# Performance work log

Measured on AMD Instinct MI355X. Metric: run time of the kernel, lower is better.

The kernel has to match this reference:

```python
import math
import jax, jax.numpy as jnp
import numpy as np

TWO_PI = 2.0 * math.pi


def cyclic_catmull_rom(phase, num_cp):
    """Returns (indices [B,4] int32, weights [B,4] float)."""
    pos = jnp.remainder(phase, TWO_PI) * (num_cp / TWO_PI)
    base = jnp.floor(pos).astype(jnp.int32)
    t = pos - base.astype(pos.dtype)
    t2 = t * t
    t3 = t2 * t
    idx = jnp.stack([
        jnp.remainder(base - 1, num_cp),
        jnp.remainder(base, num_cp),
        jnp.remainder(base + 1, num_cp),
        jnp.remainder(base + 2, num_cp),
    ], axis=1)
    w = jnp.stack([
        -0.5 * t + t2 - 0.5 * t3,
        1.0 - 2.5 * t2 + 1.5 * t3,
        0.5 * t + 2.0 * t2 - 1.5 * t3,
        -0.5 * t2 + 0.5 * t3,
    ], axis=1)
    return idx, w


def setup_inputs() -> dict:
    key = jax.random.key(0)
    ks = jax.random.split(key, 10)
    B = 16384
    INPUT_DIM = 33          # phase + 32 state features
    STATE = 32
    EXP = 128               # expanded_input_dim
    PN = 8                  # phase_node_count
    C = 8                   # phase_control_points
    H1, H2 = 256, 256
    OUT = 16
    FIRST_IN = EXP + PN + STATE          # 168
    PF_IN = H1 + STATE                   # 288

    def xavier(k, shape):
        fan_out, fan_in = shape[-2], shape[-1]
        lim = math.sqrt(6.0 / (fan_in + fan_out))
        return jax.random.uniform(k, shape, jnp.float32, -lim, lim)

    return {
        "inputs": jax.random.normal(ks[0], (B, INPUT_DIM), jnp.float32),
        "exp_w": xavier(ks[1], (EXP, STATE)),
        "exp_b": jnp.zeros((EXP,), jnp.float32),
        "phase_node_cp": 0.02 * jax.random.normal(ks[2], (C, PN), jnp.float32),
        "w1": xavier(ks[3], (H1, FIRST_IN)),
        "b1": jnp.zeros((H1,), jnp.float32),
        "pf_w": xavier(ks[4], (C, H2, PF_IN)),
        "pf_b": jnp.zeros((C, H2), jnp.float32),
        "w_out": xavier(ks[5], (OUT, H2 + STATE)),
        "b_out": jnp.zeros((OUT,), jnp.float32),
    }


def reference(inputs, exp_w, exp_b, phase_node_cp, w1, b1, pf_w, pf_b, w_out, b_out):
    num_cp = pf_w.shape[0]
    phase = inputs[:, 0]
    state = inputs[:, 1:]                                  # [B, S]

    expanded = jax.nn.elu(state @ exp_w.T + exp_b)          # [B, EXP]

    idx, w = cyclic_catmull_rom(phase, num_cp)              # [B,4], [B,4]
    phase_nodes = jnp.sum(w[:, :, None] * phase_node_cp[idx], axis=1)  # [B, PN]

    h1 = jax.nn.elu(jnp.concatenate([expanded, phase_nodes, state], axis=1) @ w1.T + b1)
    h2_in = jnp.concatenate([h1, state], axis=1)            # [B, PF_IN]

    # Phase-functioned linear: compute matvec against every control matrix,
    # then gather + blend the 4 relevant ones (same math as blending weight
    # matrices first, by linearity; avoids the [B,4,OUT,IN] intermediate).
    z = jnp.einsum('bi,coi->bco', h2_in, pf_w)              # [B, C, H2]
    z4 = jnp.take_along_axis(z, idx[:, :, None], axis=1)    # [B, 4, H2]
    b4 = pf_b[idx]                                          # [B, 4, H2]
    h2 = jax.nn.elu(jnp.sum(w[:, :, None] * (z4 + b4), axis=1))

    return jnp.concatenate([h2, state], axis=1) @ w_out.T + b_out
```

## Files before the change

### kernel.cpp

```cpp
#include <hip/hip_runtime.h>
#include <math.h>

typedef short bf16x8 __attribute__((ext_vector_type(8)));
typedef float f32x4 __attribute__((ext_vector_type(4)));

#define MFMA16(a, b, c) __builtin_amdgcn_mfma_f32_16x16x32_bf16((a), (b), (c), 0, 0, 0)

#define TWO_PI_F 6.28318530717958647692f

#define PFW_OFF    0
#define PFW_ELEMS  (8 * 2 * 8 * 9 * 512)
#define W1_OFF     (PFW_OFF + PFW_ELEMS)
#define W1_ELEMS   (16 * 6 * 512)
#define EXPW_OFF   (W1_OFF + W1_ELEMS)
#define EXPW_ELEMS (8 * 512)
#define WOUT_OFF   (EXPW_OFF + EXPW_ELEMS)
#define WOUT_ELEMS (9 * 512)
#define TOTAL_ELEMS (WOUT_OFF + WOUT_ELEMS)

#define MAIN_THREADS 512
#define TILE_B 64

__device__ __forceinline__ unsigned short f2bf(float x) {
    unsigned int u = __float_as_uint(x);
    unsigned int r = u + 0x7fffu + ((u >> 16) & 1u);
    return (unsigned short)(r >> 16);
}

__device__ __forceinline__ float elu_f(float x) {
    return x > 0.0f ? x : (expf(x) - 1.0f);
}

__global__ __launch_bounds__(256) void prep_weights(
    const float* __restrict__ exp_w, const float* __restrict__ w1,
    const float* __restrict__ pf_w, const float* __restrict__ w_out,
    unsigned short* __restrict__ wsb)
{
    int i = blockIdx.x * blockDim.x + threadIdx.x;
    if (i >= TOTAL_ELEMS) return;
    float v;
    if (i < W1_OFF) {
        int f = i >> 9, e512 = i & 511;
        int ln = e512 >> 3, e = e512 & 7;
        int kgp = ln >> 4, cf = ln & 15;
        int kk = f % 9; int rest = f / 9;
        int n_t = rest & 7; int rest2 = rest >> 3;
        int half = rest2 & 1; int c = rest2 >> 1;
        int n = half * 128 + n_t * 16 + cf;
        int k = kk * 32 + kgp * 8 + e;
        v = pf_w[((size_t)(c * 256 + n)) * 288 + k];
    } else if (i < EXPW_OFF) {
        int j = i - W1_OFF;
        int f = j >> 9, e512 = j & 511;
        int ln = e512 >> 3, e = e512 & 7;
        int kgp = ln >> 4, cf = ln & 15;
        int kk = f % 6; int n16 = f / 6;
        int n = n16 * 16 + cf;
        int k = kk * 32 + kgp * 8 + e;
        v = (k < 168) ? w1[n * 168 + k] : 0.0f;
    } else if (i < WOUT_OFF) {
        int j = i - EXPW_OFF;
        int n16 = j >> 9; int e512 = j & 511;
        int ln = e512 >> 3, e = e512 & 7;
        int kgp = ln >> 4, cf = ln & 15;
        v = exp_w[(n16 * 16 + cf) * 32 + kgp * 8 + e];
    } else {
        int j = i - WOUT_OFF;
        int kk = j >> 9; int e512 = j & 511;
        int ln = e512 >> 3, e = e512 & 7;
        int kgp = ln >> 4, cf = ln & 15;
        int k = kk * 32 + kgp * 8 + e;
        v = w_out[cf * 288 + k];
    }
    wsb[i] = f2bf(v);
}

__global__ __launch_bounds__(MAIN_THREADS, 2) void pfnn_mfma(
    const float* __restrict__ inputs,
    const float* __restrict__ exp_b,
    const float* __restrict__ cp,
    const float* __restrict__ b1,
    const float* __restrict__ pf_b,
    const float* __restrict__ b_out,
    const unsigned short* __restrict__ wsb,
    float* __restrict__ out, int B)
{
    __shared__ __align__(16) unsigned short buf1[TILE_B * 296];
    __shared__ __align__(16) unsigned short buf2[TILE_B * 296];
    __shared__ float sWcT[8][TILE_B];

    const unsigned short* pfwb  = wsb + PFW_OFF;
    const unsigned short* w1b   = wsb + W1_OFF;
    const unsigned short* expwb = wsb + EXPW_OFF;
    const unsigned short* woutb = wsb + WOUT_OFF;

    const int t    = threadIdx.x;
    const int w    = t >> 6;
    const int lane = t & 63;
    const int cfr  = lane & 15;
    const int kg   = lane >> 4;
    const int b0   = blockIdx.x * TILE_B;

    for (int i = t; i < TILE_B * 32; i += MAIN_THREADS) {
        int row = i >> 5, j = i & 31;
        int grow = b0 + row;
        float v = (grow < B) ? inputs[(size_t)grow * 33 + 1 + j] : 0.0f;
        unsigned short bv = f2bf(v);
        buf1[row * 296 + 136 + j] = bv;
        buf1[row * 296 + 256 + j] = bv;
        buf2[row * 296 + 256 + j] = bv;
        buf1[row * 296 + 168 + j] = 0;
    }
    if (t < TILE_B) {
        int grow = b0 + t;
        float ph = (grow < B) ? inputs[(size_t)grow * 33] : 0.0f;
        float p = fmodf(ph, TWO_PI_F);
        if (p < 0.0f) p += TWO_PI_F;
        float pos = p * (8.0f / TWO_PI_F);
        int base = (int)floorf(pos);
        float tt = pos - (float)base;
        base &= 7;
        float t2 = tt * tt, t3 = t2 * tt;
        float cw0 = -0.5f * tt + t2 - 0.5f * t3;
        float cw1 = 1.0f - 2.5f * t2 + 1.5f * t3;
        float cw2 = 0.5f * tt + 2.0f * t2 - 1.5f * t3;
        float cw3 = -0.5f * t2 + 0.5f * t3;
        int i0 = (base + 7) & 7, i1 = base, i2 = (base + 1) & 7, i3 = (base + 2) & 7;
        #pragma unroll
        for (int c = 0; c < 8; ++c) sWcT[c][t] = 0.0f;
        sWcT[i0][t] += cw0;
        sWcT[i1][t] += cw1;
        sWcT[i2][t] += cw2;
        sWcT[i3][t] += cw3;
        #pragma unroll
        for (int j = 0; j < 8; ++j) {
            float pn = cw0 * cp[i0 * 8 + j] + cw1 * cp[i1 * 8 + j]
                     + cw2 * cp[i2 * 8 + j] + cw3 * cp[i3 * 8 + j];
            buf1[t * 296 + 128 + j] = f2bf(pn);
        }
    }
    __syncthreads();

    {
        const int n0 = w * 16;
        bf16x8 bw = *(const bf16x8*)(expwb + w * 512 + lane * 8);
        const f32x4 zero = {0.f, 0.f, 0.f, 0.f};
        f32x4 acc[4];
        #pragma unroll
        for (int m = 0; m < 4; ++m) {
            bf16x8 a = *(const bf16x8*)&buf1[(m * 16 + cfr) * 296 + 136 + kg * 8];
            acc[m] = MFMA16(a, bw, zero);
        }
        float bias = exp_b[n0 + cfr];
        #pragma unroll
        for (int m = 0; m < 4; ++m)
            #pragma unroll
            for (int r = 0; r < 4; ++r) {
                int row = m * 16 + kg * 4 + r;
                buf1[row * 296 + n0 + cfr] = f2bf(elu_f(acc[m][r] + bias));
            }
    }
    __syncthreads();

    {
        const int n0 = w * 32;
        f32x4 acc[2][4];
        #pragma unroll
        for (int nt = 0; nt < 2; ++nt)
            #pragma unroll
            for (int m = 0; m < 4; ++m)
                acc[nt][m] = (f32x4){0.f, 0.f, 0.f, 0.f};
        #pragma unroll
        for (int kk = 0; kk < 6; ++kk) {
            bf16x8 a[4];
            #pragma unroll
            for (int m = 0; m < 4; ++m)
                a[m] = *(const bf16x8*)&buf1[(m * 16 + cfr) * 296 + kk * 32 + kg * 8];
            #pragma unroll
            for (int nt = 0; nt < 2; ++nt) {
                bf16x8 bw = *(const bf16x8*)(w1b + ((w * 2 + nt) * 6 + kk) * 512 + lane * 8);
                #pragma unroll
                for (int m = 0; m < 4; ++m)
                    acc[nt][m] = MFMA16(a[m], bw, acc[nt][m]);
            }
        }
        #pragma unroll
        for (int nt = 0; nt < 2; ++nt) {
            float bias = b1[n0 + nt * 16 + cfr];
            #pragma unroll
            for (int m = 0; m < 4; ++m)
                #pragma unroll
                for (int r = 0; r < 4; ++r) {
                    int row = m * 16 + kg * 4 + r;
                    buf2[row * 296 + n0 + nt * 16 + cfr] = f2bf(elu_f(acc[nt][m][r] + bias));
                }
        }
    }
    __syncthreads();

    {
        const int n0 = w * 32;
        const int g0 = w * 2;
        const size_t fb0 = (size_t)(((g0 >> 3) * 8 + (g0 & 7)) * 9) * 512 + lane * 8;
        const size_t fb1 = (size_t)((((g0 + 1) >> 3) * 8 + ((g0 + 1) & 7)) * 9) * 512 + lane * 8;

        f32x4 h2acc[2][4];
        #pragma unroll
        for (int nt = 0; nt < 2; ++nt)
            #pragma unroll
            for (int m = 0; m < 4; ++m)
                h2acc[nt][m] = (f32x4){0.f, 0.f, 0.f, 0.f};

        for (int c = 0; c < 8; ++c) {
            const unsigned short* wp0 = pfwb + (size_t)(c * 2 * 8 * 9) * 512 + fb0;
            const unsigned short* wp1 = pfwb + (size_t)(c * 2 * 8 * 9) * 512 + fb1;

            f32x4 z[2][4];
            #pragma unroll
            for (int nt = 0; nt < 2; ++nt)
                #pragma unroll
                for (int m = 0; m < 4; ++m)
                    z[nt][m] = (f32x4){0.f, 0.f, 0.f, 0.f};

            #pragma unroll
            for (int kk = 0; kk < 9; ++kk) {
                bf16x8 bw0 = *(const bf16x8*)(wp0 + kk * 512);
                bf16x8 bw1 = *(const bf16x8*)(wp1 + kk * 512);
                #pragma unroll
                for (int m = 0; m < 4; ++m) {
                    bf16x8 a = *(const bf16x8*)&buf2[(m * 16 + cfr) * 296 + kk * 32 + kg * 8];
                    z[0][m] = MFMA16(a, bw0, z[0][m]);
                    z[1][m] = MFMA16(a, bw1, z[1][m]);
                }
            }

            float pfb0 = pf_b[c * 256 + n0 + cfr];
            float pfb1 = pf_b[c * 256 + n0 + 16 + cfr];
            #pragma unroll
            for (int m = 0; m < 4; ++m) {
                f32x4 wcv = *(const f32x4*)&sWcT[c][m * 16 + kg * 4];
                #pragma unroll
                for (int r = 0; r < 4; ++r) {
                    h2acc[0][m][r] += wcv[r] * (z[0][m][r] + pfb0);
                    h2acc[1][m][r] += wcv[r] * (z[1][m][r] + pfb1);
                }
            }
        }
        #pragma unroll
        for (int nt = 0; nt < 2; ++nt)
            #pragma unroll
            for (int m = 0; m < 4; ++m)
                #pragma unroll
                for (int r = 0; r < 4; ++r) {
                    int row = m * 16 + kg * 4 + r;
                    buf1[row * 296 + n0 + nt * 16 + cfr] = f2bf(elu_f(h2acc[nt][m][r]));
                }
    }
    __syncthreads();

    if (w < 4) {
        f32x4 acc = {0.f, 0.f, 0.f, 0.f};
        #pragma unroll
        for (int kk = 0; kk < 9; ++kk) {
            bf16x8 a  = *(const bf16x8*)&buf1[(w * 16 + cfr) * 296 + kk * 32 + kg * 8];
            bf16x8 bw = *(const bf16x8*)(woutb + kk * 512 + lane * 8);
            acc = MFMA16(a, bw, acc);
        }
        float bias = b_out[cfr];
        #pragma unroll
        for (int r = 0; r < 4; ++r) {
            int grow = b0 + w * 16 + kg * 4 + r;
            if (grow < B) out[(size_t)grow * 16 + cfr] = acc[r] + bias;
        }
    }
}

#define FB_TILE 16
#define FB_THREADS 256

__global__ __launch_bounds__(FB_THREADS) void pfnn_fused_f32(
    const float* __restrict__ inputs,
    const float* __restrict__ exp_w, const float* __restrict__ exp_b,
    const float* __restrict__ cp,
    const float* __restrict__ w1, const float* __restrict__ b1,
    const float* __restrict__ pf_w, const float* __restrict__ pf_b,
    const float* __restrict__ w_out, const float* __restrict__ b_out,
    float* __restrict__ out, int B)
{
    __shared__ float sState[FB_TILE][36];
    __shared__ float sFI[FB_TILE][172];
    __shared__ float sH2in[FB_TILE][292];
    __shared__ float sH2[FB_TILE][260];
    __shared__ float sWc[FB_TILE][8];
    __shared__ float sPhase[FB_TILE];

    const int t = threadIdx.x;
    const int b0 = blockIdx.x * FB_TILE;
    const int nb = min(FB_TILE, B - b0);

    for (int i = t; i < nb * 33; i += FB_THREADS) {
        int b = i / 33, j = i % 33;
        float v = inputs[(size_t)(b0 + b) * 33 + j];
        if (j == 0) sPhase[b] = v;
        else { sState[b][j-1] = v; sFI[b][136 + j-1] = v; sH2in[b][256 + j-1] = v; }
    }
    for (int i = nb * 33 + t; i < FB_TILE * 33; i += FB_THREADS) {
        int b = i / 33, j = i % 33;
        if (j == 0) sPhase[b] = 0.0f;
        else { sState[b][j-1] = 0.0f; sFI[b][136 + j-1] = 0.0f; sH2in[b][256 + j-1] = 0.0f; }
    }
    __syncthreads();
    {
        const int o = t & 127;
        const int bh = t >> 7;
        const float4* wrow = reinterpret_cast<const float4*>(exp_w + o * 32);
        float4 wv[8];
        #pragma unroll
        for (int q = 0; q < 8; ++q) wv[q] = wrow[q];
        const float bias = exp_b[o];
        for (int bi = bh; bi < FB_TILE; bi += 2) {
            float acc = bias;
            #pragma unroll
            for (int q = 0; q < 8; ++q) {
                acc += wv[q].x * sState[bi][q*4+0] + wv[q].y * sState[bi][q*4+1]
                     + wv[q].z * sState[bi][q*4+2] + wv[q].w * sState[bi][q*4+3];
            }
            sFI[bi][o] = elu_f(acc);
        }
    }
    if (t < FB_TILE) {
        float p = fmodf(sPhase[t], TWO_PI_F);
        if (p < 0.0f) p += TWO_PI_F;
        float pos = p * (8.0f / TWO_PI_F);
        int base = (int)floorf(pos);
        float tt = pos - (float)base;
        base &= 7;
        float t2 = tt*tt, t3 = t2*tt;
        float cw0 = -0.5f*tt + t2 - 0.5f*t3;
        float cw1 = 1.0f - 2.5f*t2 + 1.5f*t3;
        float cw2 = 0.5f*tt + 2.0f*t2 - 1.5f*t3;
        float cw3 = -0.5f*t2 + 0.5f*t3;
        int i0 = (base+7)&7, i1 = base, i2 = (base+1)&7, i3 = (base+2)&7;
        #pragma unroll
        for (int c = 0; c < 8; ++c) sWc[t][c] = 0.0f;
        sWc[t][i0] += cw0; sWc[t][i1] += cw1; sWc[t][i2] += cw2; sWc[t][i3] += cw3;
        #pragma unroll
        for (int j = 0; j < 8; ++j)
            sFI[t][128 + j] = cw0*cp[i0*8+j] + cw1*cp[i1*8+j] + cw2*cp[i2*8+j] + cw3*cp[i3*8+j];
    }
    __syncthreads();
    {
        const int o = t;
        float acc[FB_TILE];
        const float bias = b1[o];
        #pragma unroll
        for (int b = 0; b < FB_TILE; ++b) acc[b] = bias;
        const float* wrow = w1 + o * 168;
        for (int k4 = 0; k4 < 42; ++k4) {
            float4 wv = *reinterpret_cast<const float4*>(wrow + k4 * 4);
            #pragma unroll
            for (int b = 0; b < FB_TILE; ++b) {
                float4 a = *reinterpret_cast<const float4*>(&sFI[b][k4 * 4]);
                acc[b] += wv.x*a.x + wv.y*a.y + wv.z*a.z + wv.w*a.w;
            }
        }
        #pragma unroll
        for (int b = 0; b < FB_TILE; ++b) sH2in[b][o] = elu_f(acc[b]);
    }
    __syncthreads();
    {
        const int o = t;
        float h2acc[FB_TILE];
        #pragma unroll
        for (int b = 0; b < FB_TILE; ++b) h2acc[b] = 0.0f;
        for (int g = 0; g < 2; ++g) {
            float zacc[FB_TILE][4];
            #pragma unroll
            for (int b = 0; b < FB_TILE; ++b)
                #pragma unroll
                for (int ci = 0; ci < 4; ++ci) zacc[b][ci] = 0.0f;
            for (int k4 = 0; k4 < 72; ++k4) {
                float wv[4][4];
                #pragma unroll
                for (int ci = 0; ci < 4; ++ci) {
                    float4 v = *reinterpret_cast<const float4*>(
                        pf_w + (size_t)((g*4+ci) * 256 + o) * 288 + k4 * 4);
                    wv[ci][0]=v.x; wv[ci][1]=v.y; wv[ci][2]=v.z; wv[ci][3]=v.w;
                }
                #pragma unroll
                for (int b = 0; b < FB_TILE; ++b) {
                    float4 a = *reinterpret_cast<const float4*>(&sH2in[b][k4 * 4]);
                    #pragma unroll
                    for (int ci = 0; ci < 4; ++ci)
                        zacc[b][ci] += a.x*wv[ci][0] + a.y*wv[ci][1] + a.z*wv[ci][2] + a.w*wv[ci][3];
                }
            }
            #pragma unroll
            for (int b = 0; b < FB_TILE; ++b)
                #pragma unroll
                for (int ci = 0; ci < 4; ++ci)
                    h2acc[b] += sWc[b][g*4+ci] * (zacc[b][ci] + pf_b[(g*4+ci) * 256 + o]);
        }
        #pragma unroll
        for (int b = 0; b < FB_TILE; ++b) sH2[b][o] = elu_f(h2acc[b]);
    }
    __syncthreads();
    {
        const int b = t >> 4;
        const int j = t & 15;
        const float* wrow = w_out + j * 288;
        float acc = b_out[j];
        for (int k4 = 0; k4 < 64; ++k4) {
            float4 wv = *reinterpret_cast<const float4*>(wrow + k4 * 4);
            float4 a = *reinterpret_cast<const float4*>(&sH2[b][k4 * 4]);
            acc += wv.x*a.x + wv.y*a.y + wv.z*a.z + wv.w*a.w;
        }
        #pragma unroll
        for (int j2 = 0; j2 < 32; ++j2) acc += wrow[256 + j2] * sState[b][j2];
        if (b < nb) out[(size_t)(b0 + b) * 16 + j] = acc;
    }
}

extern "C" void kernel_launch(void* const* d_in, const int* in_sizes, int n_in,
                              void* d_out, int out_size, void* d_ws, size_t ws_size,
                              hipStream_t stream) {
    const float* inputs = (const float*)d_in[0];
    const float* exp_w  = (const float*)d_in[1];
    const float* exp_b  = (const float*)d_in[2];
    const float* cp     = (const float*)d_in[3];
    const float* w1     = (const float*)d_in[4];
    const float* b1     = (const float*)d_in[5];
    const float* pf_w   = (const float*)d_in[6];
    const float* pf_b   = (const float*)d_in[7];
    const float* w_out  = (const float*)d_in[8];
    const float* b_out  = (const float*)d_in[9];
    float* out = (float*)d_out;

    const int B = in_sizes[0] / 33;

    if (d_ws != nullptr && ws_size >= (size_t)TOTAL_ELEMS * sizeof(unsigned short)) {
        unsigned short* wsb = (unsigned short*)d_ws;
        prep_weights<<<(TOTAL_ELEMS + 255) / 256, 256, 0, stream>>>(
            exp_w, w1, pf_w, w_out, wsb);
        pfnn_mfma<<<(B + TILE_B - 1) / TILE_B, MAIN_THREADS, 0, stream>>>(
            inputs, exp_b, cp, b1, pf_b, b_out, wsb, out, B);
    } else {
        pfnn_fused_f32<<<(B + FB_TILE - 1) / FB_TILE, FB_THREADS, 0, stream>>>(
            inputs, exp_w, exp_b, cp, w1, b1, pf_w, pf_b, w_out, b_out, out, B);
    }
}
```

Measured before the change: 38.82 us.

## Split fused PFNN kernel into three stages with workspace intermediates

Replaces the single fused kernel with three kernels. The first computes the expansion, first layer and phase weights per 64-row tile and writes them to workspace. The second splits the phase-functioned layer across four blocks per tile, staging inputs through direct global-to-LDS loads. The third computes the output projection. The goal is more parallelism and occupancy in the heavy phase-function GEMM, at the cost of extra kernel launches and round trips of intermediates through global memory.

```diff
diff --git a/kernel.cpp b/kernel.cpp
--- a/kernel.cpp
+++ b/kernel.cpp
@@ -18,7 +18,6 @@
 #define WOUT_ELEMS (9 * 512)
 #define TOTAL_ELEMS (WOUT_OFF + WOUT_ELEMS)
 
-#define MAIN_THREADS 512
 #define TILE_B 64
 
 __device__ __forceinline__ unsigned short f2bf(float x) {
@@ -29,6 +28,12 @@
 
 __device__ __forceinline__ float elu_f(float x) {
     return x > 0.0f ? x : (expf(x) - 1.0f);
+}
+
+__device__ __forceinline__ void gload_lds16(const void* g, void* l) {
+    __builtin_amdgcn_global_load_lds(
+        (const __attribute__((address_space(1))) void*)g,
+        (__attribute__((address_space(3))) void*)l, 16, 0, 0);
 }
 
 __global__ __launch_bounds__(256) void prep_weights(
@@ -75,7 +80,251 @@
     wsb[i] = f2bf(v);
 }
 
-__global__ __launch_bounds__(MAIN_THREADS, 2) void pfnn_mfma(
+__global__ __launch_bounds__(512, 2) void k_a(
+    const float* __restrict__ inputs,
+    const float* __restrict__ exp_b,
+    const float* __restrict__ cp,
+    const float* __restrict__ b1,
+    const unsigned short* __restrict__ wsb,
+    unsigned short* __restrict__ x2b,
+    float* __restrict__ wcT,
+    int B)
+{
+    __shared__ __align__(16) unsigned short buf1[TILE_B * 296];
+    __shared__ __align__(16) unsigned short buf2[TILE_B * 296];
+    __shared__ float sWcT[8][TILE_B];
+
+    const unsigned short* w1b   = wsb + W1_OFF;
+    const unsigned short* expwb = wsb + EXPW_OFF;
+
+    const int t    = threadIdx.x;
+    const int w    = t >> 6;
+    const int lane = t & 63;
+    const int cfr  = lane & 15;
+    const int kg   = lane >> 4;
+    const int b0   = blockIdx.x * TILE_B;
+
+    for (int i = t; i < TILE_B * 32; i += 512) {
+        int row = i >> 5, j = i & 31;
+        int grow = b0 + row;
+        float v = (grow < B) ? inputs[(size_t)grow * 33 + 1 + j] : 0.0f;
+        unsigned short bv = f2bf(v);
+        buf1[row * 296 + 136 + j] = bv;
+        buf2[row * 296 + 256 + j] = bv;
+        buf1[row * 296 + 168 + j] = 0;
+    }
+    if (t < TILE_B) {
+        int grow = b0 + t;
+        #pragma unroll
+        for (int c = 0; c < 8; ++c) sWcT[c][t] = 0.0f;
+        if (grow < B) {
+            float ph = inputs[(size_t)grow * 33];
+            float p = fmodf(ph, TWO_PI_F);
+            if (p < 0.0f) p += TWO_PI_F;
+            float pos = p * (8.0f / TWO_PI_F);
+            int base = (int)floorf(pos);
+            float tt = pos - (float)base;
+            base &= 7;
+            float t2 = tt * tt, t3 = t2 * tt;
+            float cw0 = -0.5f * tt + t2 - 0.5f * t3;
+            float cw1 = 1.0f - 2.5f * t2 + 1.5f * t3;
+            float cw2 = 0.5f * tt + 2.0f * t2 - 1.5f * t3;
+            float cw3 = -0.5f * t2 + 0.5f * t3;
+            int i0 = (base + 7) & 7, i1 = base, i2 = (base + 1) & 7, i3 = (base + 2) & 7;
+            sWcT[i0][t] += cw0;
+            sWcT[i1][t] += cw1;
+            sWcT[i2][t] += cw2;
+            sWcT[i3][t] += cw3;
+            #pragma unroll
+            for (int j = 0; j < 8; ++j) {
+                float pn = cw0 * cp[i0 * 8 + j] + cw1 * cp[i1 * 8 + j]
+                         + cw2 * cp[i2 * 8 + j] + cw3 * cp[i3 * 8 + j];
+                buf1[t * 296 + 128 + j] = f2bf(pn);
+            }
+        } else {
+            #pragma unroll
+            for (int j = 0; j < 8; ++j) buf1[t * 296 + 128 + j] = 0;
+        }
+        #pragma unroll
+        for (int c = 0; c < 8; ++c)
+            wcT[(size_t)blockIdx.x * 512 + c * 64 + t] = sWcT[c][t];
+    }
+    __syncthreads();
+
+    {
+        const int n0 = w * 16;
+        bf16x8 bw = *(const bf16x8*)(expwb + w * 512 + lane * 8);
+        const f32x4 zero = {0.f, 0.f, 0.f, 0.f};
+        f32x4 acc[4];
+        #pragma unroll
+        for (int m = 0; m < 4; ++m) {
+            bf16x8 a = *(const bf16x8*)&buf1[(m * 16 + cfr) * 296 + 136 + kg * 8];
+            acc[m] = MFMA16(a, bw, zero);
+        }
+        float bias = exp_b[n0 + cfr];
+        #pragma unroll
+        for (int m = 0; m < 4; ++m)
+            #pragma unroll
+            for (int r = 0; r < 4; ++r) {
+                int row = m * 16 + kg * 4 + r;
+                buf1[row * 296 + n0 + cfr] = f2bf(elu_f(acc[m][r] + bias));
+            }
+    }
+    __syncthreads();
+
+    {
+        const int n0 = w * 32;
+        f32x4 acc[2][4];
+        #pragma unroll
+        for (int nt = 0; nt < 2; ++nt)
+            #pragma unroll
+            for (int m = 0; m < 4; ++m)
+                acc[nt][m] = (f32x4){0.f, 0.f, 0.f, 0.f};
+        #pragma unroll
+        for (int kk = 0; kk < 6; ++kk) {
+            bf16x8 a[4];
+            #pragma unroll
+            for (int m = 0; m < 4; ++m)
+                a[m] = *(const bf16x8*)&buf1[(m * 16 + cfr) * 296 + kk * 32 + kg * 8];
+            #pragma unroll
+            for (int nt = 0; nt < 2; ++nt) {
+                bf16x8 bw = *(const bf16x8*)(w1b + ((w * 2 + nt) * 6 + kk) * 512 + lane * 8);
+                #pragma unroll
+                for (int m = 0; m < 4; ++m)
+                    acc[nt][m] = MFMA16(a[m], bw, acc[nt][m]);
+            }
+        }
+        #pragma unroll
+        for (int nt = 0; nt < 2; ++nt) {
+            float bias = b1[n0 + nt * 16 + cfr];
+            #pragma unroll
+            for (int m = 0; m < 4; ++m)
+                #pragma unroll
+                for (int r = 0; r < 4; ++r) {
+                    int row = m * 16 + kg * 4 + r;
+                    buf2[row * 296 + n0 + nt * 16 + cfr] = f2bf(elu_f(acc[nt][m][r] + bias));
+                }
+        }
+    }
+    __syncthreads();
+
+    for (int f = w; f < 36; f += 8) {
+        int m = f / 9, kk = f - m * 9;
+        bf16x8 v = *(const bf16x8*)&buf2[(m * 16 + cfr) * 296 + kk * 32 + kg * 8];
+        *(bf16x8*)(x2b + (size_t)blockIdx.x * 18432 + f * 512 + lane * 8) = v;
+    }
+}
+
+__global__ __launch_bounds__(256, 2) void k_c(
+    const unsigned short* __restrict__ wsb,
+    const unsigned short* __restrict__ x2b,
+    const float* __restrict__ wcT,
+    const float* __restrict__ pf_b,
+    unsigned short* __restrict__ xoutb)
+{
+    __shared__ __align__(16) unsigned short sX2[36 * 512];
+    __shared__ __align__(16) float sWc[8][64];
+
+    const unsigned short* pfwb = wsb + PFW_OFF;
+    const int t    = threadIdx.x;
+    const int w    = t >> 6;
+    const int lane = t & 63;
+    const int cfr  = lane & 15;
+    const int kg   = lane >> 4;
+    const int rt   = blockIdx.x >> 2;
+    const int q    = blockIdx.x & 3;
+
+    {
+        const char* src = (const char*)(x2b + (size_t)rt * 18432);
+        char* dst = (char*)sX2;
+        #pragma unroll
+        for (int it = 0; it < 9; ++it)
+            gload_lds16(src + (it * 256 + t) * 16, dst + (it * 256 + t) * 16);
+        if (t < 128)
+            gload_lds16((const char*)(wcT + (size_t)rt * 512) + t * 16,
+                        (char*)sWc + t * 16);
+    }
+    __syncthreads();
+
+    const int g = q * 4 + w;
+    const size_t fb = (size_t)(((g >> 3) * 8 + (g & 7)) * 9) * 512 + lane * 8;
+    const int col = q * 64 + w * 16 + cfr;
+
+    f32x4 h2acc[4];
+    #pragma unroll
+    for (int m = 0; m < 4; ++m) h2acc[m] = (f32x4){0.f, 0.f, 0.f, 0.f};
+
+    for (int c = 0; c < 8; ++c) {
+        const unsigned short* wp = pfwb + (size_t)(c * 2 * 8 * 9) * 512 + fb;
+        f32x4 z[4];
+        #pragma unroll
+        for (int m = 0; m < 4; ++m) z[m] = (f32x4){0.f, 0.f, 0.f, 0.f};
+        #pragma unroll
+        for (int kk = 0; kk < 9; ++kk) {
+            bf16x8 bw = *(const bf16x8*)(wp + kk * 512);
+            #pragma unroll
+            for (int m = 0; m < 4; ++m) {
+                bf16x8 a = *(const bf16x8*)&sX2[(m * 9 + kk) * 512 + lane * 8];
+                z[m] = MFMA16(a, bw, z[m]);
+            }
+        }
+        float pfb = pf_b[c * 256 + col];
+        #pragma unroll
+        for (int m = 0; m < 4; ++m) {
+            f32x4 wcv = *(const f32x4*)&sWc[c][m * 16 + kg * 4];
+            #pragma unroll
+            for (int r = 0; r < 4; ++r)
+                h2acc[m][r] += wcv[r] * (z[m][r] + pfb);
+        }
+    }
+
+    const int kkG = q * 2 + (w >> 1);
+    const int lif = ((w & 1) * 2 + (cfr >> 3)) * 16;
+    unsigned short* ob = xoutb + (size_t)rt * 16384;
+    #pragma unroll
+    for (int m = 0; m < 4; ++m)
+        #pragma unroll
+        for (int r = 0; r < 4; ++r)
+            ob[(m * 8 + kkG) * 512 + (lif + kg * 4 + r) * 8 + (cfr & 7)]
+                = f2bf(elu_f(h2acc[m][r]));
+}
+
+__global__ __launch_bounds__(256, 2) void k_d(
+    const unsigned short* __restrict__ wsb,
+    const unsigned short* __restrict__ xoutb,
+    const unsigned short* __restrict__ x2b,
+    const float* __restrict__ b_out,
+    float* __restrict__ out, int B)
+{
+    const unsigned short* woutb = wsb + WOUT_OFF;
+    const int t    = threadIdx.x;
+    const int w    = t >> 6;
+    const int lane = t & 63;
+    const int cfr  = lane & 15;
+    const int kg   = lane >> 4;
+    const int rt   = blockIdx.x;
+
+    f32x4 acc = {0.f, 0.f, 0.f, 0.f};
+    #pragma unroll
+    for (int kk = 0; kk < 8; ++kk) {
+        bf16x8 a  = *(const bf16x8*)(xoutb + (size_t)rt * 16384 + (w * 8 + kk) * 512 + lane * 8);
+        bf16x8 bw = *(const bf16x8*)(woutb + kk * 512 + lane * 8);
+        acc = MFMA16(a, bw, acc);
+    }
+    {
+        bf16x8 a  = *(const bf16x8*)(x2b + (size_t)rt * 18432 + (w * 9 + 8) * 512 + lane * 8);
+        bf16x8 bw = *(const bf16x8*)(woutb + 8 * 512 + lane * 8);
+        acc = MFMA16(a, bw, acc);
+    }
+    float bias = b_out[cfr];
+    #pragma unroll
+    for (int r = 0; r < 4; ++r) {
+        int grow = rt * 64 + w * 16 + kg * 4 + r;
+        if (grow < B) out[(size_t)grow * 16 + cfr] = acc[r] + bias;
+    }
+}
+
+__global__ __launch_bounds__(512, 2) void pfnn_mono(
     const float* __restrict__ inputs,
     const float* __restrict__ exp_b,
     const float* __restrict__ cp,
@@ -101,7 +350,7 @@
     const int kg   = lane >> 4;
     const int b0   = blockIdx.x * TILE_B;
 
-    for (int i = t; i < TILE_B * 32; i += MAIN_THREADS) {
+    for (int i = t; i < TILE_B * 32; i += 512) {
         int row = i >> 5, j = i & 31;
         int grow = b0 + row;
         float v = (grow < B) ? inputs[(size_t)grow * 33 + 1 + j] : 0.0f;
@@ -437,12 +686,30 @@
     float* out = (float*)d_out;
 
     const int B = in_sizes[0] / 33;
-
-    if (d_ws != nullptr && ws_size >= (size_t)TOTAL_ELEMS * sizeof(unsigned short)) {
+    const int ntl = (B + TILE_B - 1) / TILE_B;
+
+    const size_t wsb_e  = TOTAL_ELEMS;
+    const size_t x2_e   = (size_t)ntl * 36 * 512;
+    const size_t xo_e   = (size_t)ntl * 32 * 512;
+    const size_t need_split = (wsb_e + x2_e + xo_e) * 2 + (size_t)ntl * 512 * 4;
+    const size_t need_mono  = wsb_e * 2;
+
+    if (d_ws != nullptr && ws_size >= need_split) {
+        unsigned short* wsb   = (unsigned short*)d_ws;
+        unsigned short* x2b   = wsb + wsb_e;
+        unsigned short* xoutb = x2b + x2_e;
+        float*          wcT   = (float*)(xoutb + xo_e);
+
+        prep_weights<<<(TOTAL_ELEMS + 255) / 256, 256, 0, stream>>>(
+            exp_w, w1, pf_w, w_out, wsb);
+        k_a<<<ntl, 512, 0, stream>>>(inputs, exp_b, cp, b1, wsb, x2b, wcT, B);
+        k_c<<<ntl * 4, 256, 0, stream>>>(wsb, x2b, wcT, pf_b, xoutb);
+        k_d<<<ntl, 256, 0, stream>>>(wsb, xoutb, x2b, b_out, out, B);
+    } else if (d_ws != nullptr && ws_size >= need_mono) {
         unsigned short* wsb = (unsigned short*)d_ws;
         prep_weights<<<(TOTAL_ELEMS + 255) / 256, 256, 0, stream>>>(
             exp_w, w1, pf_w, w_out, wsb);
-        pfnn_mfma<<<(B + TILE_B - 1) / TILE_B, MAIN_THREADS, 0, stream>>>(
+        pfnn_mono<<<ntl, 512, 0, stream>>>(
             inputs, exp_b, cp, b1, pf_b, b_out, wsb, out, B);
     } else {
         pfnn_fused_f32<<<(B + FB_TILE - 1) / FB_TILE, FB_THREADS, 0, stream>>>(
```

After: 65.09 us. 1.68x slower.
